# Performance work log

Measured on AMD Instinct MI355X. Metric: run time of the kernel, lower is better.

## Reference

```python
import jax, jax.numpy as jnp
import numpy as np

DEPTH = 5
B, CHANNELS, LENGTH = 256, 10, 128


def setup_inputs() -> dict:
    key = jax.random.key(0)
    # torch module convention: (batch, channels, length); transposed internally to (length, channels)
    path = jax.random.normal(key, (B, CHANNELS, LENGTH), dtype=jnp.float32)
    return {"path": path, "depth": DEPTH}


def _seg_levels(delta, depth):
    # Signature of a single linear segment with increment delta: level k = delta^{\otimes k} / k!
    # delta: (B, d) -> list of (B, d**k) for k = 1..depth
    b = delta.shape[0]
    levels = [delta]
    cur = delta
    for k in range(2, depth + 1):
        cur = (cur[:, :, None] * delta[:, None, :]).reshape(b, -1) / k
        levels.append(cur)
    return levels


def _signature(path_ld, depth):
    # path_ld: (B, L, d) piecewise-linear path; returns (B, sum_k d**k)
    b, L, d = path_ld.shape
    inc = path_ld[:, 1:] - path_ld[:, :-1]  # (B, L-1, d) segment increments
    init = tuple(_seg_levels(inc[:, 0], depth))

    def step(carry, delta):
        # Chen's relation: (S \otimes T)_k = S_k + T_k + sum_{i=1}^{k-1} S_i \otimes T_{k-i}
        T = _seg_levels(delta, depth)
        new = []
        for k in range(1, depth + 1):
            acc = carry[k - 1] + T[k - 1]
            for i in range(1, k):
                acc = acc + (carry[i - 1][:, :, None] * T[k - i - 1][:, None, :]).reshape(b, d ** k)
            new.append(acc)
        return tuple(new), None

    deltas = jnp.swapaxes(inc[:, 1:], 0, 1)  # (L-2, B, d) remaining segments
    final, _ = jax.lax.scan(step, init, deltas)
    return jnp.concatenate(final, axis=-1)


def reference(path, depth):
    # path: (B, channels, length) as in the torch module; iisignature sees (length, channels)
    return _signature(jnp.swapaxes(path, 1, 2), depth)
```

## Files before the change

### kernel.cpp

```cpp
#include <hip/hip_runtime.h>


#define D10    10
#define LPATH  128
#define NSEG   127
#define BLOCK  256
#define KC     16
#define RS     12
#define OUT_PER_B 111110

__global__ __launch_bounds__(BLOCK) void sig_kernel(
        const float* __restrict__ path,
        float* __restrict__ out)
{
    __shared__ __align__(16) float dT[NSEG * RS];
    __shared__ float Wp1[KC * 100];
    __shared__ float Wp0[KC * 100];

    const int tid = threadIdx.x;
    const int bb  = blockIdx.x;
    const int b   = bb / 10;
    const int g   = bb - b * 10;
    const float* pb = path + (size_t)b * (D10 * LPATH);

    for (int idx = tid; idx < NSEG * D10; idx += BLOCK) {
        int t = idx / D10, c = idx - t * D10;
        dT[t * RS + c] = pb[c * LPATH + t + 1] - pb[c * LPATH + t];
    }

    const int c2 = tid / 10;
    const int c3 = tid - c2 * 10;
    int m3r[4];
#pragma unroll
    for (int r = 0; r < 4; r++) m3r[r] = (tid + 250 * r) / 10;

    float s1 = 0.f, s2 = 0.f, s3 = 0.f;
    float S4r[4] = {0.f, 0.f, 0.f, 0.f};
    float acc[4][10];
#pragma unroll
    for (int r = 0; r < 4; r++)
#pragma unroll
        for (int e = 0; e < 10; e++) acc[r][e] = 0.f;

    for (int kc0 = 0; kc0 < NSEG; kc0 += KC) {
        const int kn = (NSEG - kc0 < KC) ? (NSEG - kc0) : KC;
        __syncthreads();

        if (tid < 100) {
            for (int kl = 0; kl < kn; kl++) {
                const int t = kc0 + kl;
                float dg  = dT[t * RS + g];
                float dc2 = dT[t * RS + c2];
                float dc3 = dT[t * RS + c3];
                float u24 = s2 + (s1 + dg * 0.25f)       * dc2 * (1.f / 3.f);
                float u25 = s2 + (s1 + dg * 0.2f)        * dc2 * 0.25f;
                float u23 = s2 + (s1 + dg * (1.f / 3.f)) * dc2 * 0.5f;
                Wp1[kl * 100 + tid] = s3 + u24 * dc3 * 0.5f;
                Wp0[kl * 100 + tid] = s3 + u25 * dc3 * (1.f / 3.f);
                s3 += u23 * dc3;
                s2 += (s1 + dg * 0.5f) * dc2;
                s1 += dg;
            }
        }
        __syncthreads();

        if (tid < 250) {
            for (int kl = 0; kl < kn; kl++) {
                const int t = kc0 + kl;
                const float* dr = &dT[t * RS];
                float4 dA = *(const float4*)dr;
                float4 dB = *(const float4*)(dr + 4);
                float2 dC = *(const float2*)(dr + 8);
                float de[10] = {dA.x, dA.y, dA.z, dA.w,
                                dB.x, dB.y, dB.z, dB.w, dC.x, dC.y};
                float dc4v = dr[c3];
                float hd   = 0.5f * dc4v;
#pragma unroll
                for (int r = 0; r < 4; r++) {
                    float w1v = Wp1[kl * 100 + m3r[r]];
                    float w0v = Wp0[kl * 100 + m3r[r]];
                    float c4v = S4r[r] + w0v * hd;
                    S4r[r] += w1v * dc4v;
#pragma unroll
                    for (int e = 0; e < 10; e++) acc[r][e] += c4v * de[e];
                }
            }
        }
    }

    float* ob = out + (size_t)b * OUT_PER_B;
    if (tid < 100) {
        ob[110 + g * 100 + tid] = s3;
        if (c3 == 0) ob[10 + g * 10 + c2] = s2;
        if (tid == 0) ob[g] = s1;
    }
    if (tid < 250) {
#pragma unroll
        for (int r = 0; r < 4; r++) {
            const int j = tid + 250 * r;
            ob[1110 + g * 1000 + j] = S4r[r];
            float* o5 = ob + 11110 + (size_t)g * 10000 + (size_t)j * 10;
#pragma unroll
            for (int e = 0; e < 10; e += 2) {
                float2 vv = make_float2(acc[r][e], acc[r][e + 1]);
                *(float2*)&o5[e] = vv;
            }
        }
    }
}

extern "C" void kernel_launch(void* const* d_in, const int* in_sizes, int n_in,
                              void* d_out, int out_size, void* d_ws, size_t ws_size,
                              hipStream_t stream) {
    const float* path = (const float*)d_in[0];
    float* out = (float*)d_out;
    int B = in_sizes[0] / (D10 * LPATH);
    sig_kernel<<<B * 10, BLOCK, 0, stream>>>(path, out);
}
```

Measured before the change: 229.9 us.

## Double-buffer level-3 weights, pad segments, and fully unroll chunk loops

```diff
diff --git a/kernel.cpp b/kernel.cpp
--- a/kernel.cpp
+++ b/kernel.cpp
@@ -4,18 +4,19 @@
 #define D10    10
 #define LPATH  128
 #define NSEG   127
+#define NSEGP  128
 #define BLOCK  256
 #define KC     16
+#define NCH    8
 #define RS     12
 #define OUT_PER_B 111110
 
-__global__ __launch_bounds__(BLOCK) void sig_kernel(
+__global__ __launch_bounds__(BLOCK, 4) void sig_kernel(
         const float* __restrict__ path,
         float* __restrict__ out)
 {
-    __shared__ __align__(16) float dT[NSEG * RS];
-    __shared__ float Wp1[KC * 100];
-    __shared__ float Wp0[KC * 100];
+    __shared__ __align__(16) float dT[NSEGP * RS];
+    __shared__ __align__(16) float2 Wp[2][KC * 100];
 
     const int tid = threadIdx.x;
     const int bb  = blockIdx.x;
@@ -27,12 +28,11 @@
         int t = idx / D10, c = idx - t * D10;
         dT[t * RS + c] = pb[c * LPATH + t + 1] - pb[c * LPATH + t];
     }
+    if (tid < RS) dT[NSEG * RS + tid] = 0.f;
+    __syncthreads();
 
     const int c2 = tid / 10;
     const int c3 = tid - c2 * 10;
-    int m3r[4];
-#pragma unroll
-    for (int r = 0; r < 4; r++) m3r[r] = (tid + 250 * r) / 10;
 
     float s1 = 0.f, s2 = 0.f, s3 = 0.f;
     float S4r[4] = {0.f, 0.f, 0.f, 0.f};
@@ -42,21 +42,25 @@
 #pragma unroll
         for (int e = 0; e < 10; e++) acc[r][e] = 0.f;
 
-    for (int kc0 = 0; kc0 < NSEG; kc0 += KC) {
-        const int kn = (NSEG - kc0 < KC) ? (NSEG - kc0) : KC;
-        __syncthreads();
+    for (int ch = 0; ch < NCH; ch++) {
+        float2* wp = Wp[ch & 1];
+        const float* dbase = &dT[ch * (KC * RS)];
 
         if (tid < 100) {
-            for (int kl = 0; kl < kn; kl++) {
-                const int t = kc0 + kl;
-                float dg  = dT[t * RS + g];
-                float dc2 = dT[t * RS + c2];
-                float dc3 = dT[t * RS + c3];
+            const float* drg = dbase + g;
+            const float* dr2 = dbase + c2;
+            const float* dr3 = dbase + c3;
+            float2* wpo = wp + tid;
+#pragma unroll
+            for (int kl = 0; kl < KC; kl++) {
+                float dg  = drg[kl * RS];
+                float dc2 = dr2[kl * RS];
+                float dc3 = dr3[kl * RS];
                 float u24 = s2 + (s1 + dg * 0.25f)       * dc2 * (1.f / 3.f);
                 float u25 = s2 + (s1 + dg * 0.2f)        * dc2 * 0.25f;
                 float u23 = s2 + (s1 + dg * (1.f / 3.f)) * dc2 * 0.5f;
-                Wp1[kl * 100 + tid] = s3 + u24 * dc3 * 0.5f;
-                Wp0[kl * 100 + tid] = s3 + u25 * dc3 * (1.f / 3.f);
+                wpo[kl * 100] = make_float2(s3 + u24 * dc3 * 0.5f,
+                                            s3 + u25 * dc3 * (1.f / 3.f));
                 s3 += u23 * dc3;
                 s2 += (s1 + dg * 0.5f) * dc2;
                 s1 += dg;
@@ -65,22 +69,23 @@
         __syncthreads();
 
         if (tid < 250) {
-            for (int kl = 0; kl < kn; kl++) {
-                const int t = kc0 + kl;
-                const float* dr = &dT[t * RS];
+            const float2* wb = wp + c2;
+            const float*  dc = dbase + c3;
+#pragma unroll
+            for (int kl = 0; kl < KC; kl++) {
+                const float* dr = dbase + kl * RS;
                 float4 dA = *(const float4*)dr;
                 float4 dB = *(const float4*)(dr + 4);
                 float2 dC = *(const float2*)(dr + 8);
                 float de[10] = {dA.x, dA.y, dA.z, dA.w,
                                 dB.x, dB.y, dB.z, dB.w, dC.x, dC.y};
-                float dc4v = dr[c3];
+                float dc4v = dc[kl * RS];
                 float hd   = 0.5f * dc4v;
 #pragma unroll
                 for (int r = 0; r < 4; r++) {
-                    float w1v = Wp1[kl * 100 + m3r[r]];
-                    float w0v = Wp0[kl * 100 + m3r[r]];
-                    float c4v = S4r[r] + w0v * hd;
-                    S4r[r] += w1v * dc4v;
+                    float2 w = wb[kl * 100 + 25 * r];
+                    float c4v = S4r[r] + w.y * hd;
+                    S4r[r] += w.x * dc4v;
 #pragma unroll
                     for (int e = 0; e < 10; e++) acc[r][e] += c4v * de[e];
                 }
```

Result: slower. 362.6 us (+57.7%).
